# Kernel tuning notes

Hardware: AMD Instinct MI355X
Metric: run time of the kernel (lower is better)

Reference implementation:

```python
import jax, jax.numpy as jnp
import numpy as np

N_SHIFT = 23          # self.n in the torch module
OUTPUT_BIT = 8
INT31_MAX = 2147483647.0  # 2**31 - 1


def floor_ste(x):
    # straight-through floor: forward floor, backward identity
    return x + jax.lax.stop_gradient(jnp.floor(x) - x)


def int_exp_shift(x_int, scaling_factor):
    # integer-only exp approximation via shift decomposition
    x_int = x_int + floor_ste(x_int / 2.0) - floor_ste(x_int / 16.0)  # x*(1+1/2-1/16) ~ x*ln2^-1 trick
    x0_int = jax.lax.stop_gradient(jnp.floor(-1.0 / scaling_factor))   # -ln2 in integer domain (no grad)
    x_int = jnp.maximum(x_int, N_SHIFT * x0_int)
    q = floor_ste(x_int / x0_int)                 # integer quotient, in [0, N_SHIFT]
    r = x_int - x0_int * q                        # remainder
    exp_int = r / 2.0 - x0_int
    exp_int = jnp.maximum(floor_ste(exp_int * jnp.exp2(N_SHIFT - q)), 0.0)
    return exp_int


def setup_inputs() -> dict:
    key = jax.random.key(0)
    k1, _ = jax.random.split(key)
    x = jax.random.normal(k1, (64, 197, 3072), dtype=jnp.float32)
    # realistic per-tensor activation quantization scale
    scaling_factor = jnp.ones((1,), dtype=jnp.float32) * 0.02
    return {"x": x, "scaling_factor": scaling_factor}


def reference(x, scaling_factor):
    pre_x_int = x / scaling_factor                      # [B, T, H] integer-domain input
    sf_sig = scaling_factor * 1.702                     # sigmoid(1.702*x) GELU approx scale
    x_int_max = jnp.max(pre_x_int, axis=-1, keepdims=True)   # [B, T, 1]
    x_int = pre_x_int - x_int_max                       # shift for numerical range
    exp_int = int_exp_shift(x_int, sf_sig)              # exp(x - m)
    exp_int_max = int_exp_shift(-x_int_max, sf_sig)     # exp(-m) == exp(0 - m)
    exp_int_sum = jnp.minimum(exp_int + exp_int_max, INT31_MAX)
    factor = floor_ste(INT31_MAX / exp_int_sum)
    sigmoid_int = floor_ste(exp_int * factor / 2.0 ** (31 - OUTPUT_BIT + 1))
    out_sf = scaling_factor * (1.0 / 2.0 ** (OUTPUT_BIT - 1))
    x_int_out = pre_x_int * sigmoid_int
    return x_int_out * out_sf, out_sf
```

## Files before the change

### kernel.cpp

```cpp
#include <hip/hip_runtime.h>
#include <math.h>


#define ROWLEN   3072
#define NTHREADS 256

typedef float f32x4 __attribute__((ext_vector_type(4)));

__device__ __forceinline__ float crdiv(float a, float b, float y) {
    #pragma clang fp contract(off)
    float q0 = a * y;
    float r  = fmaf(-q0, b, a);
    return fmaf(r, y, q0);
}

__device__ __forceinline__ float int_exp_fast(float xi, float x0, float y_x0,
                                              float c23x0) {
    #pragma clang fp contract(off)
    float t = (xi + floorf(xi * 0.5f)) - floorf(xi * 0.0625f);
    t = fmaxf(t, c23x0);
    float q = floorf(t * y_x0);
    float r = t - x0 * q;
    float e = r * 0.5f - x0;
    e = floorf(ldexpf(e, 23 - (int)q));
    return fmaxf(e, 0.0f);
}

__device__ __forceinline__ float int_exp_cr(float xi, float x0, float y_x0,
                                            float c23x0) {
    #pragma clang fp contract(off)
    float t = (xi + floorf(xi * 0.5f)) - floorf(xi * 0.0625f);
    t = fmaxf(t, c23x0);
    float q = floorf(crdiv(t, x0, y_x0));
    float r = t - x0 * q;
    float e = r * 0.5f - x0;
    e = floorf(ldexpf(e, 23 - (int)q));
    return fmaxf(e, 0.0f);
}

__global__ __launch_bounds__(NTHREADS)
void intgelu_kernel(const float* __restrict__ x, const float* __restrict__ sfp,
                    float* __restrict__ out, long long scalar_idx) {
    #pragma clang fp contract(off)
    const int row = blockIdx.x;
    const int tid = threadIdx.x;

    const float sf     = sfp[0];
    const float y_sf   = 1.0f / sf;
    const float x0     = floorf(-1.0f / (sf * 1.702f));
    const float y_x0   = 1.0f / x0;
    const float c23x0  = 23.0f * x0;
    const float out_sf = sf * 0.0078125f;

    const float* xr   = x   + (size_t)row * ROWLEN;
    float*       outr = out + (size_t)row * ROWLEN;

    float p[12];
    float lmax = -INFINITY;
    #pragma unroll
    for (int c = 0; c < 3; ++c) {
        float4 v = reinterpret_cast<const float4*>(xr)[c * NTHREADS + tid];
        lmax = fmaxf(lmax, fmaxf(fmaxf(v.x, v.y), fmaxf(v.z, v.w)));
        p[c*4+0] = crdiv(v.x, sf, y_sf);
        p[c*4+1] = crdiv(v.y, sf, y_sf);
        p[c*4+2] = crdiv(v.z, sf, y_sf);
        p[c*4+3] = crdiv(v.w, sf, y_sf);
    }

    #pragma unroll
    for (int off = 32; off > 0; off >>= 1)
        lmax = fmaxf(lmax, __shfl_xor(lmax, off, 64));
    __shared__ float smax[NTHREADS / 64];
    if ((tid & 63) == 0) smax[tid >> 6] = lmax;
    __syncthreads();
    const float mraw = fmaxf(fmaxf(smax[0], smax[1]), fmaxf(smax[2], smax[3]));

    const float m  = crdiv(mraw, sf, y_sf);
    const float em = int_exp_cr(0.0f - m, x0, y_x0, c23x0);

    #pragma unroll
    for (int c = 0; c < 3; ++c) {
        f32x4 o;
        #pragma unroll
        for (int j = 0; j < 4; ++j) {
            float pp = p[c*4+j];
            float e  = int_exp_fast(pp - m, x0, y_x0, c23x0);
            float s  = e + em;
            float f  = floorf(2147483648.0f / s);
            float sg = floorf((e * f) * 5.9604644775390625e-8f);
            o[j] = (pp * sg) * out_sf;
        }
        reinterpret_cast<f32x4*>(outr)[c * NTHREADS + tid] = o;
    }

    if (row == 0 && tid == 0) out[scalar_idx] = out_sf;
}

extern "C" void kernel_launch(void* const* d_in, const int* in_sizes, int n_in,
                              void* d_out, int out_size, void* d_ws, size_t ws_size,
                              hipStream_t stream) {
    const float* x   = (const float*)d_in[0];
    const float* sfp = (const float*)d_in[1];
    float*       out = (float*)d_out;
    const int nrows  = in_sizes[0] / ROWLEN;
    const long long scalar_idx = (long long)out_size - 1;
    intgelu_kernel<<<nrows, NTHREADS, 0, stream>>>(x, sfp, out, scalar_idx);
}
```

Before: 265.3 us.

## Assign one wavefront per row to drop block-level reduction and barrier

Each 64-lane wavefront now owns a full row of 3072 floats, loading 12 float4 vectors per lane, so the row max needs only a wavefront shuffle reduction and no shared memory or __syncthreads. All loads are issued up front before any compute, which raises memory-level parallelism per thread. The cost is higher register pressure (48 floats per lane plus temporaries), which may lower occupancy. Grid size is divided by four and assumes the row count is divisible by four (12608 rows is).

```diff
diff --git a/kernel.cpp b/kernel.cpp
--- a/kernel.cpp
+++ b/kernel.cpp
@@ -4,6 +4,7 @@
 
 #define ROWLEN   3072
 #define NTHREADS 256
+#define VPT      12
 
 typedef float f32x4 __attribute__((ext_vector_type(4)));
 
@@ -42,8 +43,9 @@
 void intgelu_kernel(const float* __restrict__ x, const float* __restrict__ sfp,
                     float* __restrict__ out, long long scalar_idx) {
     #pragma clang fp contract(off)
-    const int row = blockIdx.x;
-    const int tid = threadIdx.x;
+    const int tid  = threadIdx.x;
+    const int lane = tid & 63;
+    const int row  = blockIdx.x * (NTHREADS / 64) + (tid >> 6);
 
     const float sf     = sfp[0];
     const float y_sf   = 1.0f / sf;
@@ -52,48 +54,49 @@
     const float c23x0  = 23.0f * x0;
     const float out_sf = sf * 0.0078125f;
 
-    const float* xr   = x   + (size_t)row * ROWLEN;
-    float*       outr = out + (size_t)row * ROWLEN;
+    const f32x4* xr = reinterpret_cast<const f32x4*>(x + (size_t)row * ROWLEN);
 
-    float p[12];
+    f32x4 v[VPT];
+    #pragma unroll
+    for (int c = 0; c < VPT; ++c)
+        v[c] = xr[c * 64 + lane];
+
     float lmax = -INFINITY;
     #pragma unroll
-    for (int c = 0; c < 3; ++c) {
-        float4 v = reinterpret_cast<const float4*>(xr)[c * NTHREADS + tid];
-        lmax = fmaxf(lmax, fmaxf(fmaxf(v.x, v.y), fmaxf(v.z, v.w)));
-        p[c*4+0] = crdiv(v.x, sf, y_sf);
-        p[c*4+1] = crdiv(v.y, sf, y_sf);
-        p[c*4+2] = crdiv(v.z, sf, y_sf);
-        p[c*4+3] = crdiv(v.w, sf, y_sf);
-    }
+    for (int c = 0; c < VPT; ++c)
+        lmax = fmaxf(lmax, fmaxf(fmaxf(v[c][0], v[c][1]), fmaxf(v[c][2], v[c][3])));
 
     #pragma unroll
     for (int off = 32; off > 0; off >>= 1)
         lmax = fmaxf(lmax, __shfl_xor(lmax, off, 64));
-    __shared__ float smax[NTHREADS / 64];
-    if ((tid & 63) == 0) smax[tid >> 6] = lmax;
-    __syncthreads();
-    const float mraw = fmaxf(fmaxf(smax[0], smax[1]), fmaxf(smax[2], smax[3]));
 
-    const float m  = crdiv(mraw, sf, y_sf);
+    #pragma unroll
+    for (int c = 0; c < VPT; ++c) {
+        v[c][0] = crdiv(v[c][0], sf, y_sf);
+        v[c][1] = crdiv(v[c][1], sf, y_sf);
+        v[c][2] = crdiv(v[c][2], sf, y_sf);
+        v[c][3] = crdiv(v[c][3], sf, y_sf);
+    }
+    const float m  = crdiv(lmax, sf, y_sf);
     const float em = int_exp_cr(0.0f - m, x0, y_x0, c23x0);
 
+    f32x4* outr = reinterpret_cast<f32x4*>(out + (size_t)row * ROWLEN);
     #pragma unroll
-    for (int c = 0; c < 3; ++c) {
+    for (int c = 0; c < VPT; ++c) {
         f32x4 o;
         #pragma unroll
         for (int j = 0; j < 4; ++j) {
-            float pp = p[c*4+j];
+            float pp = v[c][j];
             float e  = int_exp_fast(pp - m, x0, y_x0, c23x0);
             float s  = e + em;
             float f  = floorf(2147483648.0f / s);
             float sg = floorf((e * f) * 5.9604644775390625e-8f);
             o[j] = (pp * sg) * out_sf;
         }
-        reinterpret_cast<f32x4*>(outr)[c * NTHREADS + tid] = o;
+        outr[c * 64 + lane] = o;
     }
 
-    if (row == 0 && tid == 0) out[scalar_idx] = out_sf;
+    if (row == 0 && lane == 0) out[scalar_idx] = out_sf;
 }
 
 extern "C" void kernel_launch(void* const* d_in, const int* in_sizes, int n_in,
@@ -104,5 +107,6 @@
     float*       out = (float*)d_out;
     const int nrows  = in_sizes[0] / ROWLEN;
     const long long scalar_idx = (long long)out_size - 1;
-    intgelu_kernel<<<nrows, NTHREADS, 0, stream>>>(x, sfp, out, scalar_idx);
+    const int grid = nrows / (NTHREADS / 64);
+    intgelu_kernel<<<grid, NTHREADS, 0, stream>>>(x, sfp, out, scalar_idx);
 }
```

After: 270.8 us. 2.1% more time.

## Split row max into a separate kernel and re-read input in main pass

Applied to the files above, without the earlier changes.

Computes the per-row max in a dedicated kernel, one wavefront per row, writing to workspace. The main kernel then reads that max and streams the input again without the block-wide reduction or barrier. This removes the in-kernel sync and the register staging of the whole row, but adds a second full read of the input (about 155 MB) and an extra launch. Since the original fused kernel was memory bound, the extra traffic probably costs more than the sync it saves.

```diff
diff --git a/kernel.cpp b/kernel.cpp
--- a/kernel.cpp
+++ b/kernel.cpp
@@ -39,8 +39,29 @@
 }
 
 __global__ __launch_bounds__(NTHREADS)
+void rowmax_kernel(const float* __restrict__ x, float* __restrict__ mraw,
+                   int nrows) {
+    const int lane = threadIdx.x & 63;
+    const int row  = blockIdx.x * (NTHREADS / 64) + (threadIdx.x >> 6);
+    if (row >= nrows) return;
+
+    const f32x4* xr = reinterpret_cast<const f32x4*>(x + (size_t)row * ROWLEN);
+    float lmax = -INFINITY;
+    #pragma unroll
+    for (int c = 0; c < 12; ++c) {
+        f32x4 v = xr[c * 64 + lane];
+        lmax = fmaxf(lmax, fmaxf(fmaxf(v[0], v[1]), fmaxf(v[2], v[3])));
+    }
+    #pragma unroll
+    for (int off = 32; off > 0; off >>= 1)
+        lmax = fmaxf(lmax, __shfl_xor(lmax, off, 64));
+    if (lane == 0) mraw[row] = lmax;
+}
+
+__global__ __launch_bounds__(NTHREADS)
 void intgelu_kernel(const float* __restrict__ x, const float* __restrict__ sfp,
-                    float* __restrict__ out, long long scalar_idx) {
+                    const float* __restrict__ mraw, float* __restrict__ out,
+                    long long scalar_idx) {
     #pragma clang fp contract(off)
     const int row = blockIdx.x;
     const int tid = threadIdx.x;
@@ -52,45 +73,26 @@
     const float c23x0  = 23.0f * x0;
     const float out_sf = sf * 0.0078125f;
 
-    const float* xr   = x   + (size_t)row * ROWLEN;
-    float*       outr = out + (size_t)row * ROWLEN;
+    const float m  = crdiv(mraw[row], sf, y_sf);
+    const float em = int_exp_cr(0.0f - m, x0, y_x0, c23x0);
 
-    float p[12];
-    float lmax = -INFINITY;
-    #pragma unroll
-    for (int c = 0; c < 3; ++c) {
-        float4 v = reinterpret_cast<const float4*>(xr)[c * NTHREADS + tid];
-        lmax = fmaxf(lmax, fmaxf(fmaxf(v.x, v.y), fmaxf(v.z, v.w)));
-        p[c*4+0] = crdiv(v.x, sf, y_sf);
-        p[c*4+1] = crdiv(v.y, sf, y_sf);
-        p[c*4+2] = crdiv(v.z, sf, y_sf);
-        p[c*4+3] = crdiv(v.w, sf, y_sf);
-    }
-
-    #pragma unroll
-    for (int off = 32; off > 0; off >>= 1)
-        lmax = fmaxf(lmax, __shfl_xor(lmax, off, 64));
-    __shared__ float smax[NTHREADS / 64];
-    if ((tid & 63) == 0) smax[tid >> 6] = lmax;
-    __syncthreads();
-    const float mraw = fmaxf(fmaxf(smax[0], smax[1]), fmaxf(smax[2], smax[3]));
-
-    const float m  = crdiv(mraw, sf, y_sf);
-    const float em = int_exp_cr(0.0f - m, x0, y_x0, c23x0);
+    const f32x4* xr   = reinterpret_cast<const f32x4*>(x   + (size_t)row * ROWLEN);
+    f32x4*       outr = reinterpret_cast<f32x4*>(out + (size_t)row * ROWLEN);
 
     #pragma unroll
     for (int c = 0; c < 3; ++c) {
+        f32x4 v = xr[c * NTHREADS + tid];
         f32x4 o;
         #pragma unroll
         for (int j = 0; j < 4; ++j) {
-            float pp = p[c*4+j];
+            float pp = crdiv(v[j], sf, y_sf);
             float e  = int_exp_fast(pp - m, x0, y_x0, c23x0);
             float s  = e + em;
             float f  = floorf(2147483648.0f / s);
             float sg = floorf((e * f) * 5.9604644775390625e-8f);
             o[j] = (pp * sg) * out_sf;
         }
-        reinterpret_cast<f32x4*>(outr)[c * NTHREADS + tid] = o;
+        outr[c * NTHREADS + tid] = o;
     }
 
     if (row == 0 && tid == 0) out[scalar_idx] = out_sf;
@@ -102,7 +104,11 @@
     const float* x   = (const float*)d_in[0];
     const float* sfp = (const float*)d_in[1];
     float*       out = (float*)d_out;
+    float*       mraw = (float*)d_ws;
     const int nrows  = in_sizes[0] / ROWLEN;
     const long long scalar_idx = (long long)out_size - 1;
-    intgelu_kernel<<<nrows, NTHREADS, 0, stream>>>(x, sfp, out, scalar_idx);
+
+    const int grid1 = (nrows + (NTHREADS / 64) - 1) / (NTHREADS / 64);
+    rowmax_kernel<<<grid1, NTHREADS, 0, stream>>>(x, mraw, nrows);
+    intgelu_kernel<<<nrows, NTHREADS, 0, stream>>>(x, sfp, mraw, out, scalar_idx);
 }
```

Result: slower. 286.9 us (+8.2%).
